# Kernel optimization log

Hardware: AMD Instinct MI355X
Metric: run time of the kernel (lower is better)

The kernel has to match this reference:

```python
import jax, jax.numpy as jnp
import numpy as np

EPS = 1e-10

def _mlp(x, W1, b1, W2, b2):
    # Linear -> ReLU -> Linear (matches _MultiLayerPercep)
    return jnp.maximum(x @ W1 + b1, 0.0) @ W2 + b2

def setup_inputs() -> dict:
    key = jax.random.key(0)
    ks = jax.random.split(key, 24)
    B, P, Q, P2, D = 512, 100, 40, 40, 64
    Nu, Ni, Nr = 100000, 100000, 6

    def lin(k, fi, fo):
        kw, kb = jax.random.split(k)
        s = 1.0 / np.sqrt(fi)
        return (jax.random.uniform(kw, (fi, fo), jnp.float32, -s, s),
                jax.random.uniform(kb, (fo,), jnp.float32, -s, s))

    uids = jax.random.randint(ks[0], (B,), 0, Nu)
    u_item_pad = jnp.stack([jax.random.randint(ks[1], (B, P), 0, Ni),
                            jax.random.randint(ks[2], (B, P), 0, Nr)], axis=-1)
    u_user_pad = jax.random.randint(ks[3], (B, Q), 0, Nu)
    u_user_item_pad = jnp.stack([jax.random.randint(ks[4], (B, Q, P2), 0, Ni),
                                 jax.random.randint(ks[5], (B, Q, P2), 0, Nr)], axis=-1)

    user_table = jax.random.normal(ks[6], (Nu, D), jnp.float32) * 0.1
    item_table = jax.random.normal(ks[7], (Ni, D), jnp.float32) * 0.1
    rate_table = jax.random.normal(ks[8], (Nr, D), jnp.float32) * 0.1

    gv_W1, gv_b1 = lin(ks[9], 2 * D, D)
    gv_W2, gv_b2 = lin(ks[10], D, D)
    atti_W1, atti_b1 = lin(ks[11], 2 * D, D)
    atti_W2, atti_b2 = lin(ks[12], D, 1)
    agg_W, agg_b = lin(ks[13], D, D)
    attu_W1, attu_b1 = lin(ks[14], 2 * D, D)
    attu_W2, attu_b2 = lin(ks[15], D, 1)
    aggn_W, aggn_b = lin(ks[16], D, D)
    cm_W1, cm_b1 = lin(ks[17], 2 * D, D)
    cm_W2, cm_b2 = lin(ks[18], D, D)
    cm_W3, cm_b3 = lin(ks[19], D, D)

    return dict(uids=uids, u_item_pad=u_item_pad, u_user_pad=u_user_pad,
                u_user_item_pad=u_user_item_pad,
                user_table=user_table, item_table=item_table, rate_table=rate_table,
                gv_W1=gv_W1, gv_b1=gv_b1, gv_W2=gv_W2, gv_b2=gv_b2,
                atti_W1=atti_W1, atti_b1=atti_b1, atti_W2=atti_W2, atti_b2=atti_b2,
                agg_W=agg_W, agg_b=agg_b,
                attu_W1=attu_W1, attu_b1=attu_b1, attu_W2=attu_W2, attu_b2=attu_b2,
                aggn_W=aggn_W, aggn_b=aggn_b,
                cm_W1=cm_W1, cm_b1=cm_b1, cm_W2=cm_W2, cm_b2=cm_b2, cm_W3=cm_W3, cm_b3=cm_b3)

def reference(uids, u_item_pad, u_user_pad, u_user_item_pad,
              user_table, item_table, rate_table,
              gv_W1, gv_b1, gv_W2, gv_b2,
              atti_W1, atti_b1, atti_W2, atti_b2,
              agg_W, agg_b,
              attu_W1, attu_b1, attu_W2, attu_b2,
              aggn_W, aggn_b,
              cm_W1, cm_b1, cm_W2, cm_b2, cm_W3, cm_b3):
    f32 = jnp.float32

    # ---- item aggregation branch ----
    q_a = item_table[u_item_pad[:, :, 0]]                      # [B,P,D]
    mask_u = (u_item_pad[:, :, 0] > 0).astype(f32)             # [B,P]
    er = rate_table[u_item_pad[:, :, 1]]                       # [B,P,D]
    x_ia = _mlp(jnp.concatenate([q_a, er], -1), gv_W1, gv_b1, gv_W2, gv_b2)
    p_i = mask_u[..., None] * user_table[uids][:, None, :]     # [B,P,D]
    alpha = _mlp(jnp.concatenate([x_ia, p_i], -1), atti_W1, atti_b1, atti_W2, atti_b2)[..., 0]
    alpha = jnp.exp(alpha) * mask_u
    alpha = alpha / (jnp.sum(alpha, axis=1, keepdims=True) + EPS)
    h_iI = jnp.maximum(jnp.sum(alpha[..., None] * x_ia, axis=1) @ agg_W + agg_b, 0.0)  # [B,D]

    # ---- social branch: per-neighbor item aggregation ----
    q_a_s = item_table[u_user_item_pad[:, :, :, 0]]            # [B,Q,P2,D]
    mask_s = (u_user_item_pad[:, :, :, 0] > 0).astype(f32)     # [B,Q,P2]
    er_s = rate_table[u_user_item_pad[:, :, :, 1]]
    x_ia_s = _mlp(jnp.concatenate([q_a_s, er_s], -1), gv_W1, gv_b1, gv_W2, gv_b2)
    nbr_emb = user_table[u_user_pad]                           # [B,Q,D]
    p_i_s = mask_s[..., None] * nbr_emb[:, :, None, :]
    alpha_s = _mlp(jnp.concatenate([x_ia_s, p_i_s], -1), atti_W1, atti_b1, atti_W2, atti_b2)[..., 0]
    alpha_s = jnp.exp(alpha_s) * mask_s
    alpha_s = alpha_s / (jnp.sum(alpha_s, axis=2, keepdims=True) + EPS)
    h_oI = jnp.maximum(jnp.sum(alpha_s[..., None] * x_ia_s, axis=2) @ agg_W + agg_b, 0.0)  # [B,Q,D]

    # ---- social attention over neighbors ----
    beta = _mlp(jnp.concatenate([h_oI, nbr_emb], -1), attu_W1, attu_b1, attu_W2, attu_b2)[..., 0]
    mask_su = (u_user_pad > 0).astype(f32)
    beta = jnp.exp(beta) * mask_su
    beta = beta / (jnp.sum(beta, axis=1, keepdims=True) + EPS)
    h_iS = jnp.maximum(jnp.sum(beta[..., None] * h_oI, axis=1) @ aggn_W + aggn_b, 0.0)  # [B,D]

    # ---- combine ----
    h = jnp.maximum(jnp.concatenate([h_iI, h_iS], -1) @ cm_W1 + cm_b1, 0.0)
    h = jnp.maximum(h @ cm_W2 + cm_b2, 0.0)
    h = jnp.maximum(h @ cm_W3 + cm_b3, 0.0)
    return h
```

## Files before the change

kernel.cpp:

```cpp
#include <hip/hip_runtime.h>
#include <math.h>

#define EPSV 1e-10f

typedef _Float16 f16x8 __attribute__((ext_vector_type(8)));
typedef _Float16 f16x4 __attribute__((ext_vector_type(4)));
typedef float f32x4 __attribute__((ext_vector_type(4)));

#define OFF_W1T  0
#define OFF_W2T  16384
#define OFF_M2T  24576
#define OFF_X    32768
#define OFF_V    49152
#define SMEM_SZ  54272

__device__ __forceinline__ f16x8 cvt_f16x8(const float4 a, const float4 b) {
  f16x8 h;
  h[0] = (_Float16)a.x; h[1] = (_Float16)a.y; h[2] = (_Float16)a.z; h[3] = (_Float16)a.w;
  h[4] = (_Float16)b.x; h[5] = (_Float16)b.y; h[6] = (_Float16)b.z; h[7] = (_Float16)b.w;
  return h;
}

__global__ __launch_bounds__(256, 2) void agg_kernel(
    const int nSblk,
    const int* __restrict__ idsS, const int* __restrict__ uidS,
    const int* __restrict__ idsI, const int* __restrict__ uidI,
    const float* __restrict__ user_table, const float* __restrict__ item_table,
    const float* __restrict__ rate_table,
    const float* __restrict__ gv_W1, const float* __restrict__ gv_b1,
    const float* __restrict__ gv_W2, const float* __restrict__ gv_b2,
    const float* __restrict__ atti_W1, const float* __restrict__ atti_b1,
    const float* __restrict__ atti_W2, const float* __restrict__ atti_b2,
    const float* __restrict__ agg_W, const float* __restrict__ agg_b,
    float* __restrict__ outS, float* __restrict__ outI) {
  __shared__ __align__(16) char smem[SMEM_SZ];
  const int tid = threadIdx.x;
  const int wave = tid >> 6, lane = tid & 63;
  const int quad = lane >> 4, mrow = lane & 15;

  const bool isS = (int)blockIdx.x < nSblk;
  const int NG = isS ? 16 : 4;
  const int P = isS ? 40 : 100;
  const int nGrp = isS ? 4 : 1;
  const int tpg = isS ? 3 : 8;
  const int* __restrict__ ids = isS ? idsS : idsI;
  const int* __restrict__ uidp = isS ? uidS : uidI;
  float* __restrict__ out = isS ? outS : outI;
  const int gbase = isS ? (int)blockIdx.x * 16 : ((int)blockIdx.x - nSblk) * 4;

  float* sV = (float*)(smem + OFF_V);
  char* smX = smem + OFF_X;
  char* smXw = smX + wave * 4096;
  float* csW = (float*)smXw;

  {
    float* uS = (float*)smX;
    float* AU = (float*)(smem + OFF_W1T);
    for (int t = tid; t < NG * 64; t += 256) {
      const int g = t >> 6, f = t & 63;
      uS[t] = user_table[(size_t)uidp[gbase + g] * 64 + f];
    }
    for (int o = tid; o < 1024; o += 256) {
      const int k = o >> 4, fb = o & 15;
      const float4 v = ((const float4*)(atti_W1 + (64 + k) * 64))[fb];
      const float* vp = (const float*)&v;
#pragma unroll
      for (int c = 0; c < 4; ++c) {
        const int j = fb * 4 + c;
        AU[j * 64 + (((k >> 2) ^ (j & 15)) << 2) + (k & 3)] = vp[c];
      }
    }
  }
  __syncthreads();
  {
    const float4* u4 = (const float4*)smX;
    const float4* a4 = (const float4*)(smem + OFF_W1T);
    for (int t = tid; t < NG * 64; t += 256) {
      const int g = t >> 6, j = t & 63;
      float s = 0.f;
#pragma unroll 4
      for (int kb = 0; kb < 16; ++kb) {
        const float4 uu = u4[g * 16 + kb];
        const float4 aa = a4[j * 16 + (kb ^ (j & 15))];
        s += uu.x * aa.x + uu.y * aa.y + uu.z * aa.z + uu.w * aa.w;
      }
      sV[t] = s;
    }
  }
  __syncthreads();
  {
    for (int o = tid; o < 2048; o += 256) {
      const int k = o >> 4, fb = o & 15;
      const float4 v = ((const float4*)(gv_W1 + k * 64))[fb];
      const float* vp = (const float*)&v;
#pragma unroll
      for (int c = 0; c < 4; ++c) {
        const int n = fb * 4 + c;
        *(_Float16*)(smem + OFF_W1T + n * 256 + ((((k >> 3) ^ (n & 7))) << 4) +
                     ((k & 7) << 1)) = (_Float16)vp[c];
      }
    }
    for (int o = tid; o < 1024; o += 256) {
      const int h = o >> 4, fb = o & 15;
      const float4 v = ((const float4*)(gv_W2 + h * 64))[fb];
      const float* vp = (const float*)&v;
#pragma unroll
      for (int c = 0; c < 4; ++c) {
        const int n = fb * 4 + c;
        *(_Float16*)(smem + OFF_W2T + n * 128 + ((((h >> 3) ^ (n & 7))) << 4) +
                     ((h & 7) << 1)) = (_Float16)vp[c];
      }
    }
    float* sCstP = (float*)smX;
    const int n = tid & 63, jh = tid >> 6;
    float p = 0.f;
#pragma unroll 4
    for (int jj = 0; jj < 16; ++jj) {
      const int j = jh * 16 + jj;
      p = fmaf(gv_b2[j], atti_W1[j * 64 + n], p);
    }
    sCstP[jh * 64 + n] = p;
  }
  float b1r[16], b2v[4], aw2v[4];
#pragma unroll
  for (int nt = 0; nt < 4; ++nt) {
#pragma unroll
    for (int rg = 0; rg < 4; ++rg) b1r[nt * 4 + rg] = gv_b1[nt * 16 + quad * 4 + rg];
    b2v[nt] = gv_b2[nt * 16 + mrow];
    aw2v[nt] = atti_W2[nt * 16 + mrow];
  }
  const float ab2 = atti_b2[0];

  float4 pf[8];
  float pm;
  auto do_prefetch = [&](int gi2, int tt2) {
    const int g2 = gbase + wave + 4 * gi2;
    const int it = tt2 * 16 + mrow;
    int iid = 0, rid = 0;
    float m = 0.f;
    if (it < P) {
      const int2 pr = ((const int2*)ids)[(size_t)g2 * P + it];
      iid = pr.x; rid = pr.y;
      m = pr.x > 0 ? 1.f : 0.f;
    }
    pm = m;
    const float* ib = item_table + (size_t)iid * 64 + quad * 8;
    const float* rb = rate_table + (size_t)rid * 64 + quad * 8;
    pf[0] = ((const float4*)ib)[0];        pf[1] = ((const float4*)ib)[1];
    pf[2] = ((const float4*)(ib + 32))[0]; pf[3] = ((const float4*)(ib + 32))[1];
    pf[4] = ((const float4*)rb)[0];        pf[5] = ((const float4*)rb)[1];
    pf[6] = ((const float4*)(rb + 32))[0]; pf[7] = ((const float4*)(rb + 32))[1];
  };
  do_prefetch(0, 0);
  __syncthreads();
  float cstv[4];
  {
    f16x8 aM[2];
#pragma unroll
    for (int ks = 0; ks < 2; ++ks) {
      f16x8 t;
#pragma unroll
      for (int j = 0; j < 8; ++j)
        t[j] = (_Float16)atti_W1[(ks * 32 + quad * 8 + j) * 64 + (wave * 16 + mrow)];
      aM[ks] = t;
    }
#pragma unroll
    for (int ht = 0; ht < 4; ++ht) {
      f32x4 c = {0.f, 0.f, 0.f, 0.f};
#pragma unroll
      for (int ks = 0; ks < 2; ++ks) {
        const float* s = gv_W2 + (ht * 16 + mrow) * 64 + ks * 32 + quad * 8;
        f16x8 b;
#pragma unroll
        for (int j = 0; j < 8; ++j) b[j] = (_Float16)s[j];
        c = __builtin_amdgcn_mfma_f32_16x16x32_f16(aM[ks], b, c, 0, 0, 0);
      }
      const int h = ht * 16 + mrow;
#pragma unroll
      for (int rg = 0; rg < 4; ++rg) {
        const int n3 = wave * 16 + quad * 4 + rg;
        *(_Float16*)(smem + OFF_M2T + n3 * 128 + ((((h >> 3) ^ (n3 & 7))) << 4) +
                     ((h & 7) << 1)) = (_Float16)c[rg];
      }
    }
    const float* sCstP = (const float*)smX;
#pragma unroll
    for (int nt = 0; nt < 4; ++nt) {
      const int n = nt * 16 + mrow;
      cstv[nt] = atti_b1[n] + sCstP[n] + sCstP[64 + n] + sCstP[128 + n] +
                 sCstP[192 + n];
    }
  }
  __syncthreads();

  f16x8 aW[4][4], bMr[4][2];
#pragma unroll
  for (int nt = 0; nt < 4; ++nt) {
#pragma unroll
    for (int ks = 0; ks < 4; ++ks)
      aW[nt][ks] = *(const f16x8*)(smem + OFF_W1T + (nt * 16 + mrow) * 256 +
                                   (((ks * 4 + quad) ^ (mrow & 7)) << 4));
#pragma unroll
    for (int ks = 0; ks < 2; ++ks)
      bMr[nt][ks] = *(const f16x8*)(smem + OFF_M2T + (nt * 16 + mrow) * 128 +
                                    (((ks * 4 + quad) ^ (mrow & 7)) << 4));
  }

  for (int gi = 0; gi < nGrp; ++gi) {
    const int g = wave + 4 * gi;
    float vv[4];
#pragma unroll
    for (int nt = 0; nt < 4; ++nt) vv[nt] = sV[g * 64 + nt * 16 + mrow];
    float pnum[4] = {0.f, 0.f, 0.f, 0.f};
    float pden = 0.f;
    for (int tt = 0; tt < tpg; ++tt) {
      f16x8 bIn[4];
      bIn[0] = cvt_f16x8(pf[0], pf[1]);
      bIn[1] = cvt_f16x8(pf[2], pf[3]);
      bIn[2] = cvt_f16x8(pf[4], pf[5]);
      bIn[3] = cvt_f16x8(pf[6], pf[7]);
      const float mcur = pm;
      {
        int ngi = gi, ntt = tt + 1;
        if (ntt == tpg) { ntt = 0; ngi = gi + 1; }
        if (ngi < nGrp) do_prefetch(ngi, ntt);
      }
#pragma unroll
      for (int nt = 0; nt < 4; ++nt) {
        f32x4 c = {0.f, 0.f, 0.f, 0.f};
#pragma unroll
        for (int ks = 0; ks < 4; ++ks)
          c = __builtin_amdgcn_mfma_f32_16x16x32_f16(aW[nt][ks], bIn[ks], c, 0, 0, 0);
        f16x4 hv;
#pragma unroll
        for (int rg = 0; rg < 4; ++rg)
          hv[rg] = (_Float16)fmaxf(c[rg] + b1r[nt * 4 + rg], 0.f);
        *(f16x4*)(smXw + mrow * 256 +
                  (((nt * 2 + (quad >> 1)) ^ (mrow & 7)) << 4) +
                  ((quad & 1) << 3)) = hv;
      }
      f16x8 a2[2];
#pragma unroll
      for (int ks = 0; ks < 2; ++ks)
        a2[ks] = *(const f16x8*)(smXw + mrow * 256 +
                                 (((ks * 4 + quad) ^ (mrow & 7)) << 4));
      float mk[4];
#pragma unroll
      for (int rg = 0; rg < 4; ++rg) mk[rg] = __shfl(mcur, quad * 4 + rg);
      f32x4 x2a[4];
      float tl[4] = {0.f, 0.f, 0.f, 0.f};
#pragma unroll
      for (int nt = 0; nt < 4; ++nt) {
        f32x4 c = {0.f, 0.f, 0.f, 0.f}, d = {0.f, 0.f, 0.f, 0.f};
#pragma unroll
        for (int ks = 0; ks < 2; ++ks) {
          const f16x8 bW = *(const f16x8*)(smem + OFF_W2T + (nt * 16 + mrow) * 128 +
                                           (((ks * 4 + quad) ^ (mrow & 7)) << 4));
          c = __builtin_amdgcn_mfma_f32_16x16x32_f16(a2[ks], bW, c, 0, 0, 0);
        }
#pragma unroll
        for (int ks = 0; ks < 2; ++ks)
          d = __builtin_amdgcn_mfma_f32_16x16x32_f16(a2[ks], bMr[nt][ks], d, 0, 0, 0);
#pragma unroll
        for (int rg = 0; rg < 4; ++rg) x2a[nt][rg] = c[rg] + b2v[nt];
#pragma unroll
        for (int rg = 0; rg < 4; ++rg) {
          const float hh = fmaxf(d[rg] + cstv[nt] + mk[rg] * vv[nt], 0.f);
          tl[rg] = fmaf(hh, aw2v[nt], tl[rg]);
        }
      }
      float e[4];
#pragma unroll
      for (int rg = 0; rg < 4; ++rg) {
        float t = tl[rg];
        t += __shfl_xor(t, 1); t += __shfl_xor(t, 2);
        t += __shfl_xor(t, 4); t += __shfl_xor(t, 8);
        e[rg] = __expf(t + ab2) * mk[rg];
        pden += e[rg];
      }
#pragma unroll
      for (int nt = 0; nt < 4; ++nt) {
        pnum[nt] = fmaf(e[0], x2a[nt][0], pnum[nt]);
        pnum[nt] = fmaf(e[1], x2a[nt][1], pnum[nt]);
        pnum[nt] = fmaf(e[2], x2a[nt][2], pnum[nt]);
        pnum[nt] = fmaf(e[3], x2a[nt][3], pnum[nt]);
      }
    }
    float dsum = pden;
    dsum += __shfl_xor(dsum, 16); dsum += __shfl_xor(dsum, 32);
    const float rd = 1.f / (dsum + EPSV);
#pragma unroll
    for (int nt = 0; nt < 4; ++nt) {
      float s = pnum[nt];
      s += __shfl_xor(s, 16); s += __shfl_xor(s, 32);
      if (quad == 0) csW[nt * 16 + mrow] = s * rd;
    }
    float acc = agg_b[lane];
#pragma unroll 8
    for (int k = 0; k < 64; ++k) acc = fmaf(csW[k], agg_W[k * 64 + lane], acc);
    out[(size_t)(gbase + g) * 64 + lane] = fmaxf(acc, 0.f);
  }
}

#define S2_W1T 0
#define S2_X   17408
#define S2_E   26112
#define S2_MSK 26240
#define S2_HB  26368
#define S2_SZ  27904

__global__ __launch_bounds__(128, 2) void stage2_kernel(
    const int* __restrict__ u_user_pad, const float* __restrict__ user_table,
    const float* __restrict__ hoI, const float* __restrict__ hiI,
    const float* __restrict__ attu_W1, const float* __restrict__ attu_b1,
    const float* __restrict__ attu_W2, const float* __restrict__ attu_b2,
    const float* __restrict__ aggn_W, const float* __restrict__ aggn_b,
    const float* __restrict__ cm_W1, const float* __restrict__ cm_b1,
    const float* __restrict__ cm_W2, const float* __restrict__ cm_b2,
    const float* __restrict__ cm_W3, const float* __restrict__ cm_b3,
    float* __restrict__ out) {
  __shared__ __align__(16) char smem[S2_SZ];
  const int tid = threadIdx.x;
  const int wave = tid >> 6, lane = tid & 63;
  const int quad = lane >> 4, mrow = lane & 15;
  const int b = (int)blockIdx.x * 2 + wave;

  char* sW1 = smem + S2_W1T;
  char* sXw = smem + S2_X + wave * 4352;
  float* sE = (float*)(smem + S2_E) + wave * 16;
  float* sM = (float*)(smem + S2_MSK) + wave * 16;
  float* sB = (float*)(smem + S2_HB) + wave * 192;

  for (int o = tid; o < 2048; o += 128) {
    const int k = o >> 4, fb = o & 15;
    const float4 v = ((const float4*)(attu_W1 + k * 64))[fb];
    const float* vp = (const float*)&v;
#pragma unroll
    for (int c = 0; c < 4; ++c) {
      const int n = fb * 4 + c;
      *(_Float16*)(sW1 + n * 272 + ((k >> 3) << 4) + ((k & 7) << 1)) = (_Float16)vp[c];
    }
  }
  float b1v[4], w2v[4];
#pragma unroll
  for (int nt = 0; nt < 4; ++nt) {
    b1v[nt] = attu_b1[nt * 16 + mrow];
    w2v[nt] = attu_W2[nt * 16 + mrow];
  }
  const float b2s = attu_b2[0];

  float4 pa[4], pb[4];
  float msk[4];
  auto pf = [&](int tt) {
#pragma unroll
    for (int k = 0; k < 4; ++k) {
      const int u = lane + (k << 6);
      const int r = u >> 4, bb = u & 15;
      const int q = tt * 16 + r;
      const int qc = q < 40 ? q : 39;
      int uid = 0;
      float m = 0.f;
      if (q < 40) {
        uid = u_user_pad[b * 40 + q];
        m = uid > 0 ? 1.f : 0.f;
      }
      msk[k] = m;
      const float* src = (bb < 8)
                             ? hoI + ((size_t)b * 40 + qc) * 64 + bb * 8
                             : user_table + (size_t)uid * 64 + (bb - 8) * 8;
      pa[k] = ((const float4*)src)[0];
      pb[k] = ((const float4*)src)[1];
    }
  };
  pf(0);
  __syncthreads();

  float numer = 0.f, pden = 0.f;
  for (int tt = 0; tt < 3; ++tt) {
#pragma unroll
    for (int k = 0; k < 4; ++k) {
      const int u = lane + (k << 6);
      const int r = u >> 4, bb = u & 15;
      *(f16x8*)(sXw + r * 272 + (bb << 4)) = cvt_f16x8(pa[k], pb[k]);
      if (bb == 0) sM[r] = msk[k];
    }
    if (tt < 2) pf(tt + 1);
    f16x8 a[4];
#pragma unroll
    for (int ks = 0; ks < 4; ++ks)
      a[ks] = *(const f16x8*)(sXw + mrow * 272 + ((ks * 4 + quad) << 4));
    float mk[4];
#pragma unroll
    for (int rg = 0; rg < 4; ++rg) mk[rg] = sM[quad * 4 + rg];
    float tl[4] = {0.f, 0.f, 0.f, 0.f};
#pragma unroll
    for (int nt = 0; nt < 4; ++nt) {
      f32x4 d = {0.f, 0.f, 0.f, 0.f};
      const int n = nt * 16 + mrow;
#pragma unroll
      for (int ks = 0; ks < 4; ++ks) {
        const f16x8 bW = *(const f16x8*)(sW1 + n * 272 + ((ks * 4 + quad) << 4));
        d = __builtin_amdgcn_mfma_f32_16x16x32_f16(a[ks], bW, d, 0, 0, 0);
      }
#pragma unroll
      for (int rg = 0; rg < 4; ++rg) {
        const float h = fmaxf(d[rg] + b1v[nt], 0.f);
        tl[rg] = fmaf(h, w2v[nt], tl[rg]);
      }
    }
    float e[4];
#pragma unroll
    for (int rg = 0; rg < 4; ++rg) {
      float t = tl[rg];
      t += __shfl_xor(t, 1); t += __shfl_xor(t, 2);
      t += __shfl_xor(t, 4); t += __shfl_xor(t, 8);
      e[rg] = __expf(t + b2s) * mk[rg];
      pden += e[rg];
    }
    if (mrow == 0) {
#pragma unroll
      for (int rg = 0; rg < 4; ++rg) sE[quad * 4 + rg] = e[rg];
    }
#pragma unroll 4
    for (int r = 0; r < 16; ++r) {
      const float er = sE[r];
      const float xv = (float)*(const _Float16*)(sXw + r * 272 + ((lane >> 3) << 4) +
                                                 ((lane & 7) << 1));
      numer = fmaf(er, xv, numer);
    }
  }
  pden += __shfl_xor(pden, 16);
  pden += __shfl_xor(pden, 32);
  const float hagg = numer / (pden + EPSV);

  sB[128 + lane] = hagg;
  sB[lane] = hiI[(size_t)b * 64 + lane];
  float acc = aggn_b[lane];
#pragma unroll 8
  for (int k = 0; k < 64; ++k) acc = fmaf(sB[128 + k], aggn_W[k * 64 + lane], acc);
  sB[64 + lane] = fmaxf(acc, 0.f);
  float c1 = cm_b1[lane];
#pragma unroll 8
  for (int k = 0; k < 128; ++k) c1 = fmaf(sB[k], cm_W1[k * 64 + lane], c1);
  sB[128 + lane] = fmaxf(c1, 0.f);
  float c2 = cm_b2[lane];
#pragma unroll 8
  for (int k = 0; k < 64; ++k) c2 = fmaf(sB[128 + k], cm_W2[k * 64 + lane], c2);
  sB[lane] = fmaxf(c2, 0.f);
  float c3 = cm_b3[lane];
#pragma unroll 8
  for (int k = 0; k < 64; ++k) c3 = fmaf(sB[k], cm_W3[k * 64 + lane], c3);
  out[(size_t)b * 64 + lane] = fmaxf(c3, 0.f);
}

extern "C" void kernel_launch(void* const* d_in, const int* in_sizes, int n_in,
                              void* d_out, int out_size, void* d_ws, size_t ws_size,
                              hipStream_t stream) {
  const int* uids = (const int*)d_in[0];
  const int* u_item_pad = (const int*)d_in[1];
  const int* u_user_pad = (const int*)d_in[2];
  const int* u_user_item_pad = (const int*)d_in[3];
  const float* user_table = (const float*)d_in[4];
  const float* item_table = (const float*)d_in[5];
  const float* rate_table = (const float*)d_in[6];
  const float* gv_W1 = (const float*)d_in[7];
  const float* gv_b1 = (const float*)d_in[8];
  const float* gv_W2 = (const float*)d_in[9];
  const float* gv_b2 = (const float*)d_in[10];
  const float* atti_W1 = (const float*)d_in[11];
  const float* atti_b1 = (const float*)d_in[12];
  const float* atti_W2 = (const float*)d_in[13];
  const float* atti_b2 = (const float*)d_in[14];
  const float* agg_W = (const float*)d_in[15];
  const float* agg_b = (const float*)d_in[16];
  const float* attu_W1 = (const float*)d_in[17];
  const float* attu_b1 = (const float*)d_in[18];
  const float* attu_W2 = (const float*)d_in[19];
  const float* attu_b2 = (const float*)d_in[20];
  const float* aggn_W = (const float*)d_in[21];
  const float* aggn_b = (const float*)d_in[22];
  const float* cm_W1 = (const float*)d_in[23];
  const float* cm_b1 = (const float*)d_in[24];
  const float* cm_W2 = (const float*)d_in[25];
  const float* cm_b2 = (const float*)d_in[26];
  const float* cm_W3 = (const float*)d_in[27];
  const float* cm_b3 = (const float*)d_in[28];
  float* out = (float*)d_out;

  float* hoI = (float*)d_ws;
  float* hiI = hoI + (size_t)512 * 40 * 64;

  agg_kernel<<<1280 + 128, 256, 0, stream>>>(
      1280, u_user_item_pad, u_user_pad, u_item_pad, uids,
      user_table, item_table, rate_table,
      gv_W1, gv_b1, gv_W2, gv_b2,
      atti_W1, atti_b1, atti_W2, atti_b2,
      agg_W, agg_b, hoI, hiI);
  stage2_kernel<<<256, 128, 0, stream>>>(u_user_pad, user_table, hoI, hiI,
                                         attu_W1, attu_b1, attu_W2, attu_b2,
                                         aggn_W, aggn_b,
                                         cm_W1, cm_b1, cm_W2, cm_b2, cm_W3, cm_b3,
                                         out);
}
```

Baseline: 292.1 us.

## Fold rate embedding into precomputed W1 rows via one-hot MFMA, double-buffer gathers

Since there are only 6 rating values, the rate_table projection through the second half of gv_W1 is precomputed into shared memory. It is then applied through a one-hot MFMA operand, so per-item rate_table gathers disappear and the first layer uses 3 K-steps instead of 4. The tile loop is flattened and alternates between two prefetch buffers, with index loads issued three tiles ahead to hide gather latency. The b2 bias add is moved out of the per-tile work into the final normalisation by scaling with dsum. This adds a one-time precompute per block and more register pressure from the double buffer.

```diff
diff --git a/kernel.cpp b/kernel.cpp
--- a/kernel.cpp
+++ b/kernel.cpp
@@ -12,7 +12,7 @@
 #define OFF_M2T  24576
 #define OFF_X    32768
 #define OFF_V    49152
-#define SMEM_SZ  54272
+#define SMEM_SZ  53248
 
 __device__ __forceinline__ f16x8 cvt_f16x8(const float4 a, const float4 b) {
   f16x8 h;
@@ -43,6 +43,7 @@
   const int P = isS ? 40 : 100;
   const int nGrp = isS ? 4 : 1;
   const int tpg = isS ? 3 : 8;
+  const int nIdx = nGrp * tpg;
   const int* __restrict__ ids = isS ? idsS : idsI;
   const int* __restrict__ uidp = isS ? uidS : uidI;
   float* __restrict__ out = isS ? outS : outI;
@@ -89,7 +90,7 @@
   }
   __syncthreads();
   {
-    for (int o = tid; o < 2048; o += 256) {
+    for (int o = tid; o < 1024; o += 256) {
       const int k = o >> 4, fb = o & 15;
       const float4 v = ((const float4*)(gv_W1 + k * 64))[fb];
       const float* vp = (const float*)&v;
@@ -110,6 +111,18 @@
         *(_Float16*)(smem + OFF_W2T + n * 128 + ((((h >> 3) ^ (n & 7))) << 4) +
                      ((h & 7) << 1)) = (_Float16)vp[c];
       }
+    }
+    for (int o = tid; o < 2048; o += 256) {
+      const int r = o >> 6, n = o & 63;
+      float s = 0.f;
+      if (r < 6) {
+#pragma unroll 8
+        for (int k = 0; k < 64; ++k)
+          s = fmaf(rate_table[r * 64 + k], gv_W1[(64 + k) * 64 + n], s);
+      }
+      *(_Float16*)(smem + OFF_W1T + n * 256 +
+                   (((8 + (r >> 3)) ^ (n & 7)) << 4) + ((r & 7) << 1)) =
+          (_Float16)s;
     }
     float* sCstP = (float*)smX;
     const int n = tid & 63, jh = tid >> 6;
@@ -131,27 +144,37 @@
   }
   const float ab2 = atti_b2[0];
 
-  float4 pf[8];
-  float pm;
-  auto do_prefetch = [&](int gi2, int tt2) {
-    const int g2 = gbase + wave + 4 * gi2;
-    const int it = tt2 * 16 + mrow;
-    int iid = 0, rid = 0;
-    float m = 0.f;
+  const int nIdxM1 = nIdx - 1;
+  int2 idreg;
+  float4 pfA[4], pfB[4];
+  float pmA, pmB;
+  int ridA, ridB;
+  auto load_ids = [&](int idx) __attribute__((always_inline)) {
+    const int ic = idx < nIdxM1 ? idx : nIdxM1;
+    const int gq = isS ? (ic * 11) >> 5 : (ic >> 3);
+    const int tt = ic - gq * tpg;
+    const int it = tt * 16 + mrow;
+    int2 pr = make_int2(0, 0);
     if (it < P) {
-      const int2 pr = ((const int2*)ids)[(size_t)g2 * P + it];
-      iid = pr.x; rid = pr.y;
-      m = pr.x > 0 ? 1.f : 0.f;
-    }
-    pm = m;
+      const int g2 = gbase + wave + 4 * gq;
+      pr = ((const int2*)ids)[(size_t)g2 * P + it];
+    }
+    idreg = pr;
+  };
+  auto issue_gather = [&](float4* pfc, float& pm0, int& rid0)
+      __attribute__((always_inline)) {
+    const int iid = idreg.x;
+    rid0 = idreg.y;
+    pm0 = iid > 0 ? 1.f : 0.f;
     const float* ib = item_table + (size_t)iid * 64 + quad * 8;
-    const float* rb = rate_table + (size_t)rid * 64 + quad * 8;
-    pf[0] = ((const float4*)ib)[0];        pf[1] = ((const float4*)ib)[1];
-    pf[2] = ((const float4*)(ib + 32))[0]; pf[3] = ((const float4*)(ib + 32))[1];
-    pf[4] = ((const float4*)rb)[0];        pf[5] = ((const float4*)rb)[1];
-    pf[6] = ((const float4*)(rb + 32))[0]; pf[7] = ((const float4*)(rb + 32))[1];
+    pfc[0] = ((const float4*)ib)[0];
+    pfc[1] = ((const float4*)ib)[1];
+    pfc[2] = ((const float4*)(ib + 32))[0];
+    pfc[3] = ((const float4*)(ib + 32))[1];
   };
-  do_prefetch(0, 0);
+  load_ids(0); issue_gather(pfA, pmA, ridA);
+  load_ids(1); issue_gather(pfB, pmB, ridB);
+  load_ids(2);
   __syncthreads();
   float cstv[4];
   {
@@ -193,11 +216,11 @@
   }
   __syncthreads();
 
-  f16x8 aW[4][4], bMr[4][2];
+  f16x8 aW[4][3], bMr[4][2];
 #pragma unroll
   for (int nt = 0; nt < 4; ++nt) {
 #pragma unroll
-    for (int ks = 0; ks < 4; ++ks)
+    for (int ks = 0; ks < 3; ++ks)
       aW[nt][ks] = *(const f16x8*)(smem + OFF_W1T + (nt * 16 + mrow) * 256 +
                                    (((ks * 4 + quad) ^ (mrow & 7)) << 4));
 #pragma unroll
@@ -206,99 +229,108 @@
                                     (((ks * 4 + quad) ^ (mrow & 7)) << 4));
   }
 
-  for (int gi = 0; gi < nGrp; ++gi) {
-    const int g = wave + 4 * gi;
-    float vv[4];
-#pragma unroll
-    for (int nt = 0; nt < 4; ++nt) vv[nt] = sV[g * 64 + nt * 16 + mrow];
-    float pnum[4] = {0.f, 0.f, 0.f, 0.f};
-    float pden = 0.f;
-    for (int tt = 0; tt < tpg; ++tt) {
-      f16x8 bIn[4];
-      bIn[0] = cvt_f16x8(pf[0], pf[1]);
-      bIn[1] = cvt_f16x8(pf[2], pf[3]);
-      bIn[2] = cvt_f16x8(pf[4], pf[5]);
-      bIn[3] = cvt_f16x8(pf[6], pf[7]);
-      const float mcur = pm;
-      {
-        int ngi = gi, ntt = tt + 1;
-        if (ntt == tpg) { ntt = 0; ngi = gi + 1; }
-        if (ngi < nGrp) do_prefetch(ngi, ntt);
-      }
+  float vv[4], pnum[4], pden = 0.f;
+  auto tile_body = [&](float4* pfc, float& pmc, int& ridc, const int idx)
+      __attribute__((always_inline)) {
+    const int gq = isS ? (idx * 11) >> 5 : (idx >> 3);
+    const int tt = idx - gq * tpg;
+    const int g = wave + 4 * gq;
+    if (tt == 0) {
 #pragma unroll
       for (int nt = 0; nt < 4; ++nt) {
-        f32x4 c = {0.f, 0.f, 0.f, 0.f};
-#pragma unroll
-        for (int ks = 0; ks < 4; ++ks)
-          c = __builtin_amdgcn_mfma_f32_16x16x32_f16(aW[nt][ks], bIn[ks], c, 0, 0, 0);
-        f16x4 hv;
-#pragma unroll
-        for (int rg = 0; rg < 4; ++rg)
-          hv[rg] = (_Float16)fmaxf(c[rg] + b1r[nt * 4 + rg], 0.f);
-        *(f16x4*)(smXw + mrow * 256 +
-                  (((nt * 2 + (quad >> 1)) ^ (mrow & 7)) << 4) +
-                  ((quad & 1) << 3)) = hv;
-      }
-      f16x8 a2[2];
+        vv[nt] = sV[g * 64 + nt * 16 + mrow];
+        pnum[nt] = 0.f;
+      }
+      pden = 0.f;
+    }
+    f16x8 bIn0 = cvt_f16x8(pfc[0], pfc[1]);
+    f16x8 bIn1 = cvt_f16x8(pfc[2], pfc[3]);
+    const float mcur = pmc;
+    const int ridcur = ridc;
+    issue_gather(pfc, pmc, ridc);
+    load_ids(idx + 3);
+    f16x8 bOne;
+#pragma unroll
+    for (int j = 0; j < 8; ++j)
+      bOne[j] = (_Float16)(quad * 8 + j == ridcur ? 1.f : 0.f);
+#pragma unroll
+    for (int nt = 0; nt < 4; ++nt) {
+      f32x4 c = {0.f, 0.f, 0.f, 0.f};
+      c = __builtin_amdgcn_mfma_f32_16x16x32_f16(aW[nt][0], bIn0, c, 0, 0, 0);
+      c = __builtin_amdgcn_mfma_f32_16x16x32_f16(aW[nt][1], bIn1, c, 0, 0, 0);
+      c = __builtin_amdgcn_mfma_f32_16x16x32_f16(aW[nt][2], bOne, c, 0, 0, 0);
+      f16x4 hv;
+#pragma unroll
+      for (int rg = 0; rg < 4; ++rg)
+        hv[rg] = (_Float16)fmaxf(c[rg] + b1r[nt * 4 + rg], 0.f);
+      *(f16x4*)(smXw + mrow * 256 +
+                (((nt * 2 + (quad >> 1)) ^ (mrow & 7)) << 4) +
+                ((quad & 1) << 3)) = hv;
+    }
+    f16x8 a2[2];
+#pragma unroll
+    for (int ks = 0; ks < 2; ++ks)
+      a2[ks] = *(const f16x8*)(smXw + mrow * 256 +
+                               (((ks * 4 + quad) ^ (mrow & 7)) << 4));
+    float mk[4];
+#pragma unroll
+    for (int rg = 0; rg < 4; ++rg) mk[rg] = __shfl(mcur, quad * 4 + rg);
+    f32x4 x2a[4];
+    float tl[4] = {0.f, 0.f, 0.f, 0.f};
+#pragma unroll
+    for (int nt = 0; nt < 4; ++nt) {
+      f32x4 c = {0.f, 0.f, 0.f, 0.f}, d = {0.f, 0.f, 0.f, 0.f};
+#pragma unroll
+      for (int ks = 0; ks < 2; ++ks) {
+        const f16x8 bW = *(const f16x8*)(smem + OFF_W2T + (nt * 16 + mrow) * 128 +
+                                         (((ks * 4 + quad) ^ (mrow & 7)) << 4));
+        c = __builtin_amdgcn_mfma_f32_16x16x32_f16(a2[ks], bW, c, 0, 0, 0);
+      }
 #pragma unroll
       for (int ks = 0; ks < 2; ++ks)
-        a2[ks] = *(const f16x8*)(smXw + mrow * 256 +
-                                 (((ks * 4 + quad) ^ (mrow & 7)) << 4));
-      float mk[4];
-#pragma unroll
-      for (int rg = 0; rg < 4; ++rg) mk[rg] = __shfl(mcur, quad * 4 + rg);
-      f32x4 x2a[4];
-      float tl[4] = {0.f, 0.f, 0.f, 0.f};
+        d = __builtin_amdgcn_mfma_f32_16x16x32_f16(a2[ks], bMr[nt][ks], d, 0, 0, 0);
+      x2a[nt] = c;
+#pragma unroll
+      for (int rg = 0; rg < 4; ++rg) {
+        const float hh = fmaxf(d[rg] + cstv[nt] + mk[rg] * vv[nt], 0.f);
+        tl[rg] = fmaf(hh, aw2v[nt], tl[rg]);
+      }
+    }
+    float e[4];
+#pragma unroll
+    for (int rg = 0; rg < 4; ++rg) {
+      float t = tl[rg];
+      t += __shfl_xor(t, 1); t += __shfl_xor(t, 2);
+      t += __shfl_xor(t, 4); t += __shfl_xor(t, 8);
+      e[rg] = __expf(t + ab2) * mk[rg];
+      pden += e[rg];
+    }
+#pragma unroll
+    for (int nt = 0; nt < 4; ++nt) {
+      pnum[nt] = fmaf(e[0], x2a[nt][0], pnum[nt]);
+      pnum[nt] = fmaf(e[1], x2a[nt][1], pnum[nt]);
+      pnum[nt] = fmaf(e[2], x2a[nt][2], pnum[nt]);
+      pnum[nt] = fmaf(e[3], x2a[nt][3], pnum[nt]);
+    }
+    if (tt == tpg - 1) {
+      float dsum = pden;
+      dsum += __shfl_xor(dsum, 16); dsum += __shfl_xor(dsum, 32);
+      const float rd = 1.f / (dsum + EPSV);
 #pragma unroll
       for (int nt = 0; nt < 4; ++nt) {
-        f32x4 c = {0.f, 0.f, 0.f, 0.f}, d = {0.f, 0.f, 0.f, 0.f};
-#pragma unroll
-        for (int ks = 0; ks < 2; ++ks) {
-          const f16x8 bW = *(const f16x8*)(smem + OFF_W2T + (nt * 16 + mrow) * 128 +
-                                           (((ks * 4 + quad) ^ (mrow & 7)) << 4));
-          c = __builtin_amdgcn_mfma_f32_16x16x32_f16(a2[ks], bW, c, 0, 0, 0);
-        }
-#pragma unroll
-        for (int ks = 0; ks < 2; ++ks)
-          d = __builtin_amdgcn_mfma_f32_16x16x32_f16(a2[ks], bMr[nt][ks], d, 0, 0, 0);
-#pragma unroll
-        for (int rg = 0; rg < 4; ++rg) x2a[nt][rg] = c[rg] + b2v[nt];
-#pragma unroll
-        for (int rg = 0; rg < 4; ++rg) {
-          const float hh = fmaxf(d[rg] + cstv[nt] + mk[rg] * vv[nt], 0.f);
-          tl[rg] = fmaf(hh, aw2v[nt], tl[rg]);
-        }
-      }
-      float e[4];
-#pragma unroll
-      for (int rg = 0; rg < 4; ++rg) {
-        float t = tl[rg];
-        t += __shfl_xor(t, 1); t += __shfl_xor(t, 2);
-        t += __shfl_xor(t, 4); t += __shfl_xor(t, 8);
-        e[rg] = __expf(t + ab2) * mk[rg];
-        pden += e[rg];
-      }
-#pragma unroll
-      for (int nt = 0; nt < 4; ++nt) {
-        pnum[nt] = fmaf(e[0], x2a[nt][0], pnum[nt]);
-        pnum[nt] = fmaf(e[1], x2a[nt][1], pnum[nt]);
-        pnum[nt] = fmaf(e[2], x2a[nt][2], pnum[nt]);
-        pnum[nt] = fmaf(e[3], x2a[nt][3], pnum[nt]);
-      }
-    }
-    float dsum = pden;
-    dsum += __shfl_xor(dsum, 16); dsum += __shfl_xor(dsum, 32);
-    const float rd = 1.f / (dsum + EPSV);
-#pragma unroll
-    for (int nt = 0; nt < 4; ++nt) {
-      float s = pnum[nt];
-      s += __shfl_xor(s, 16); s += __shfl_xor(s, 32);
-      if (quad == 0) csW[nt * 16 + mrow] = s * rd;
-    }
-    float acc = agg_b[lane];
+        float s = pnum[nt];
+        s += __shfl_xor(s, 16); s += __shfl_xor(s, 32);
+        if (quad == 0) csW[nt * 16 + mrow] = (s + b2v[nt] * dsum) * rd;
+      }
+      float acc = agg_b[lane];
 #pragma unroll 8
-    for (int k = 0; k < 64; ++k) acc = fmaf(csW[k], agg_W[k * 64 + lane], acc);
-    out[(size_t)(gbase + g) * 64 + lane] = fmaxf(acc, 0.f);
+      for (int k = 0; k < 64; ++k) acc = fmaf(csW[k], agg_W[k * 64 + lane], acc);
+      out[(size_t)(gbase + g) * 64 + lane] = fmaxf(acc, 0.f);
+    }
+  };
+  for (int idx = 0; idx < nIdx; idx += 2) {
+    tile_body(pfA, pmA, ridA, idx);
+    tile_body(pfB, pmB, ridB, idx + 1);
   }
 }
 
@@ -351,7 +383,7 @@
 
   float4 pa[4], pb[4];
   float msk[4];
-  auto pf = [&](int tt) {
+  auto pf = [&](int tt) __attribute__((always_inline)) {
 #pragma unroll
     for (int k = 0; k < 4; ++k) {
       const int u = lane + (k << 6);
```

Result: no change. 288.8 us (-1.1%).
